# Optimization experiments

Measured on AMD Instinct MI355X. Metric: run time of the kernel, lower is better.

## Reference

```python
import jax, jax.numpy as jnp
import numpy as np

# ---- configuration (from init_kwargs / image geometry) ----
NUM_CLASSES = 10          # digit classes 1..10 (scores has K+1 cols, col 0 = background)
R = 500000                # total digit proposals for the image
T = 2048                  # topk_per_image: fixed-size survivor set for jit-friendly NMS
SCORE_T = 0.05            # digit_score_thresh
NMS_T = 0.5               # nms_thresh
IMG_W, IMG_H = 1920.0, 1080.0
CLS_OFFSET = IMG_W + IMG_H + 1.0  # batched_nms coordinate-offset trick (per-class NMS)


def setup_inputs() -> dict:
    key = jax.random.key(0)
    k1, k2, k3, k4 = jax.random.split(key, 4)
    # realistic boxes: uniform centers over the image, sizes in [10, 100] px
    cxcy = jax.random.uniform(k1, (R, 2)) * jnp.array([IMG_W, IMG_H], dtype=jnp.float32)
    wh = 10.0 + 90.0 * jax.random.uniform(k2, (R, 2))
    boxes = jnp.concatenate([cxcy - 0.5 * wh, cxcy + 0.5 * wh], axis=1)  # [R,4] x1y1x2y2
    # class probabilities over K+1 classes (col 0 = background)
    scores = jax.nn.softmax(jax.random.normal(k3, (R, NUM_CLASSES + 1)), axis=1)
    # per-box digit-center score (pred_digit_center_scores)
    center_scores = jax.random.uniform(k4, (R,))
    return {"boxes": boxes, "scores": scores, "center_scores": center_scores}


def _iou_matrix(b):
    # b: [T,4] in x1y1x2y2. Returns [T,T] pairwise IoU.
    area = jnp.clip(b[:, 2] - b[:, 0], 0.0) * jnp.clip(b[:, 3] - b[:, 1], 0.0)  # [T]
    lt = jnp.maximum(b[:, None, :2], b[None, :, :2])  # [T,T,2]
    rb = jnp.minimum(b[:, None, 2:], b[None, :, 2:])  # [T,T,2]
    wh = jnp.clip(rb - lt, 0.0)
    inter = wh[..., 0] * wh[..., 1]
    return inter / (area[:, None] + area[None, :] - inter + 1e-9)


def reference(boxes, scores, center_scores):
    # 1) drop background column, fuse with digit-center scores
    fg = scores[:, 1:] * center_scores[:, None]            # [R,K]
    # 2) clip boxes to image (Boxes.clip)
    clipped = jnp.stack([
        jnp.clip(boxes[:, 0], 0.0, IMG_W),
        jnp.clip(boxes[:, 1], 0.0, IMG_H),
        jnp.clip(boxes[:, 2], 0.0, IMG_W),
        jnp.clip(boxes[:, 3], 0.0, IMG_H),
    ], axis=1)                                             # [R,4]
    # 3) flatten (box, class) candidates and threshold (filter_mask = scores > thresh)
    flat = fg.reshape(-1)                                  # [R*K]
    masked = jnp.where(flat > SCORE_T, flat, -1.0)
    # 4) fixed-size pre-filter: top-T candidates by fused score
    vals, idx = jax.lax.top_k(masked, T)                   # sorted descending
    cand_boxes = clipped[idx // NUM_CLASSES]               # [T,4]
    cand_cls = idx % NUM_CLASSES                           # [T] (cls_id - 1)
    valid = vals > SCORE_T
    # 5) per-class batched NMS via coordinate-offset trick
    nms_boxes = cand_boxes + cand_cls.astype(cand_boxes.dtype)[:, None] * CLS_OFFSET
    iou = _iou_matrix(nms_boxes)                           # [T,T]
    rng = jnp.arange(T)
    def body(i, keep):
        sup = keep[i] & (iou[i] > NMS_T) & (rng > i)
        return keep & jnp.logical_not(sup)
    keep = jax.lax.fori_loop(0, T, body, valid)            # greedy NMS (inputs sorted by score)
    # 6) masked fixed-shape outputs: kept boxes + kept scores
    out_boxes = jnp.where(keep[:, None], cand_boxes, 0.0)
    out_scores = jnp.where(keep, vals, 0.0)
    return jnp.concatenate([out_boxes, out_scores[:, None]], axis=1)  # [T,5]
```

## Files before the change

kernel.cpp:

```cpp
#include <hip/hip_runtime.h>
#include <stdint.h>

typedef unsigned int u32;
typedef unsigned long long u64;

#define SCORE_THR 0.05f
#define NMS_THR   0.5f
#define TK        2048
#define CAP       4096
#define BASE14    ((int)(0x3D4CCCCDu >> 14))
#define MAGIC11   3123612579ull
#define NREP      8
#define PAIR_CAP  16384
#define SGRID     1024

#define WS_OFFS   0
#define WS_BINPOS 16384
#define WS_HDR    32768
#define WS_CBX    33024
#define WS_NBX    65792
#define WS_VALS   98560
#define WS_HREP   106752
#define WS_BUF    237824
#define WS_PAIRS  269824

__global__ void k_hist(const float* __restrict__ scores,
                       const float* __restrict__ center,
                       int R, u32* __restrict__ hrep) {
    __shared__ u32 h[4096];
    for (int t = threadIdx.x; t < 4096; t += blockDim.x) h[t] = 0;
    __syncthreads();
    int total_e = R * 11;
    int nq = total_e >> 2;
    int qpb = (nq + (int)gridDim.x - 1) / (int)gridDim.x;
    int start = (int)blockIdx.x * qpb;
    int end = start + qpb; if (end > nq) end = nq;
    int bd = (int)blockDim.x;
    for (int q = start + (int)threadIdx.x; q < end; q += 4 * bd) {
        int q1 = q + bd, q2 = q + 2 * bd, q3 = q + 3 * bd;
        float4 va, vb, vc, vd;
        bool ga = true, gb = q1 < end, gc = q2 < end, gd = q3 < end;
        va = ((const float4*)scores)[q];
        if (gb) vb = ((const float4*)scores)[q1];
        if (gc) vc = ((const float4*)scores)[q2];
        if (gd) vd = ((const float4*)scores)[q3];
#define HPROC(g, qq, v4)                                                   \
        if (g) {                                                           \
            float vv[4] = {v4.x, v4.y, v4.z, v4.w};                        \
            _Pragma("unroll")                                              \
            for (int j = 0; j < 4; j++) {                                  \
                u32 e2 = ((u32)(qq) << 2) + (u32)j;                        \
                u32 r = (u32)(((u64)e2 * MAGIC11) >> 35);                  \
                u32 c = e2 - r * 11u;                                      \
                if (c != 0u) {                                             \
                    float s = __fmul_rn(vv[j], center[r]);                 \
                    if (s > SCORE_THR) {                                   \
                        u32 key = __float_as_uint(s);                      \
                        int b = (int)(key >> 14) - BASE14;                 \
                        b = min(max(b, 0), 4095);                          \
                        atomicAdd(&h[b], 1u);                              \
                    }                                                      \
                }                                                          \
            }                                                              \
        }
        HPROC(ga, q, va) HPROC(gb, q1, vb) HPROC(gc, q2, vc) HPROC(gd, q3, vd)
#undef HPROC
    }
    if (blockIdx.x == 0 && threadIdx.x == 0) {
        for (int e2 = nq << 2; e2 < total_e; e2++) {
            u32 r = (u32)(((u64)(u32)e2 * MAGIC11) >> 35);
            u32 c = (u32)e2 - r * 11u;
            if (c != 0u) {
                float s = __fmul_rn(scores[e2], center[r]);
                if (s > SCORE_THR) {
                    u32 key = __float_as_uint(s);
                    int b = (int)(key >> 14) - BASE14;
                    b = min(max(b, 0), 4095);
                    atomicAdd(&h[b], 1u);
                }
            }
        }
    }
    __syncthreads();
    u32* hout = hrep + (size_t)(blockIdx.x & (NREP - 1)) * 4096;
    for (int t = threadIdx.x; t < 4096; t += blockDim.x)
        if (h[t]) atomicAdd(&hout[t], h[t]);
}

__global__ void k_scan(const u32* __restrict__ hrep, u32* __restrict__ offs,
                       u32* hdr) {
    int lane = threadIdx.x;
    int base = 4096 - 64 * (lane + 1);
    u32 v[64];
    u32 segsum = 0;
#pragma unroll
    for (int j = 0; j < 64; j++) {
        u32 s = 0;
#pragma unroll
        for (int i = 0; i < NREP; i++) s += hrep[i * 4096 + base + j];
        v[j] = s; segsum += s;
    }
    u32 incl = segsum;
    for (int off = 1; off < 64; off <<= 1) {
        u32 t = (u32)__shfl_up((int)incl, off);
        if (lane >= off) incl += t;
    }
    u32 excl = incl - segsum;
    u32 total = (u32)__shfl((int)incl, 63);
    u32 run = excl;
#pragma unroll
    for (int j = 63; j >= 0; j--) { offs[base + j] = run; run += v[j]; }
    if (lane == 0) hdr[6] = total;
    if (total < (u32)TK) {
        if (lane == 0) { hdr[3] = 0; hdr[5] = total; }
        return;
    }
    if ((excl < (u32)TK) && (incl >= (u32)TK)) {
        u32 cum = excl;
#pragma unroll
        for (int j = 63; j >= 0; j--) {
            u32 nc = cum + v[j];
            if (nc >= (u32)TK) { hdr[3] = (u32)(base + j); hdr[5] = nc; break; }
            cum = nc;
        }
    }
}

__global__ void k_collect(const float* __restrict__ scores,
                          const float* __restrict__ center,
                          int R, const u32* __restrict__ hdr,
                          const u32* __restrict__ offs, u32* __restrict__ binpos,
                          u64* __restrict__ buf) {
    u32 thr = hdr[3];
    int total_e = R * 11;
    int nq = total_e >> 2;
    int qpb = (nq + (int)gridDim.x - 1) / (int)gridDim.x;
    int start = (int)blockIdx.x * qpb;
    int end = start + qpb; if (end > nq) end = nq;
    int bd = (int)blockDim.x;
    for (int q = start + (int)threadIdx.x; q < end; q += 4 * bd) {
        int q1 = q + bd, q2 = q + 2 * bd, q3 = q + 3 * bd;
        float4 va, vb, vc, vd;
        bool ga = true, gb = q1 < end, gc = q2 < end, gd = q3 < end;
        va = ((const float4*)scores)[q];
        if (gb) vb = ((const float4*)scores)[q1];
        if (gc) vc = ((const float4*)scores)[q2];
        if (gd) vd = ((const float4*)scores)[q3];
#define CPROC(g, qq, v4)                                                   \
        if (g) {                                                           \
            float vv[4] = {v4.x, v4.y, v4.z, v4.w};                        \
            _Pragma("unroll")                                              \
            for (int j = 0; j < 4; j++) {                                  \
                u32 e2 = ((u32)(qq) << 2) + (u32)j;                        \
                u32 r = (u32)(((u64)e2 * MAGIC11) >> 35);                  \
                u32 c = e2 - r * 11u;                                      \
                if (c != 0u) {                                             \
                    float s = __fmul_rn(vv[j], center[r]);                 \
                    if (s > SCORE_THR) {                                   \
                        u32 key = __float_as_uint(s);                      \
                        int b = (int)(key >> 14) - BASE14;                 \
                        b = min(max(b, 0), 4095);                          \
                        if ((u32)b >= thr) {                               \
                            u32 slot = atomicAdd(&binpos[b], 1u);          \
                            u32 pos = offs[b] + slot;                      \
                            if (pos < CAP) {                               \
                                u32 idx = r * 10u + (c - 1u);              \
                                buf[pos] = ((u64)key << 32) | (u64)(~idx); \
                            }                                              \
                        }                                                  \
                    }                                                      \
                }                                                          \
            }                                                              \
        }
        CPROC(ga, q, va) CPROC(gb, q1, vb) CPROC(gc, q2, vc) CPROC(gd, q3, vd)
#undef CPROC
    }
    if (blockIdx.x == 0 && threadIdx.x == 0) {
        for (int e2 = nq << 2; e2 < total_e; e2++) {
            u32 r = (u32)(((u64)(u32)e2 * MAGIC11) >> 35);
            u32 c = (u32)e2 - r * 11u;
            if (c != 0u) {
                float s = __fmul_rn(scores[e2], center[r]);
                if (s > SCORE_THR) {
                    u32 key = __float_as_uint(s);
                    int b = (int)(key >> 14) - BASE14;
                    b = min(max(b, 0), 4095);
                    if ((u32)b >= thr) {
                        u32 slot = atomicAdd(&binpos[b], 1u);
                        u32 pos = offs[b] + slot;
                        if (pos < CAP) {
                            u32 idx = r * 10u + (c - 1u);
                            buf[pos] = ((u64)key << 32) | (u64)(~idx);
                        }
                    }
                }
            }
        }
    }
}

__global__ __launch_bounds__(1024) void k_rank(
        const float* __restrict__ boxes, const u32* __restrict__ offs,
        const u32* __restrict__ hdr, const u64* __restrict__ buf,
        float* __restrict__ cand_bx, float* __restrict__ nms_bx,
        float* __restrict__ vals) {
    __shared__ u64 kb[CAP];
    __shared__ u32 lo[4096];
    int tid = threadIdx.x;
    u32 n = hdr[5]; if (n > (u32)CAP) n = CAP;
    u32 total = hdr[6];
    for (int t = tid; t < CAP; t += 1024) kb[t] = (t < (int)n) ? buf[t] : 0ull;
    for (int t = tid; t < 4096; t += 1024) lo[t] = offs[t];
    __syncthreads();
    for (int i = tid; i < (int)n; i += 1024) {
        u64 x = kb[i];
        u32 key = (u32)(x >> 32);
        int b = (int)(key >> 14) - BASE14;
        b = min(max(b, 0), 4095);
        u32 start = lo[b];
        u32 end = (b > 0) ? lo[b - 1] : total;
        if (end > (u32)CAP) end = CAP;
        u32 rk = start;
        for (u32 j = start; j < end; j++) rk += (kb[j] > x) ? 1u : 0u;
        if (rk < (u32)TK) {
            u32 idx = ~(u32)x;
            u32 r = idx / 10u, cls = idx % 10u;
            const float* bp = boxes + (size_t)r * 4;
            float c0 = fminf(fmaxf(bp[0], 0.f), 1920.f);
            float c1 = fminf(fmaxf(bp[1], 0.f), 1080.f);
            float c2 = fminf(fmaxf(bp[2], 0.f), 1920.f);
            float c3 = fminf(fmaxf(bp[3], 0.f), 1080.f);
            float offv = __fmul_rn((float)cls, 3001.0f);
            cand_bx[rk * 4 + 0] = c0; cand_bx[rk * 4 + 1] = c1;
            cand_bx[rk * 4 + 2] = c2; cand_bx[rk * 4 + 3] = c3;
            nms_bx[rk * 4 + 0] = __fadd_rn(c0, offv);
            nms_bx[rk * 4 + 1] = __fadd_rn(c1, offv);
            nms_bx[rk * 4 + 2] = __fadd_rn(c2, offv);
            nms_bx[rk * 4 + 3] = __fadd_rn(c3, offv);
            vals[rk] = __uint_as_float(key);
        }
    }
}

__global__ void k_mask(const float* __restrict__ nms_bx, u32* __restrict__ hdr,
                       u32* __restrict__ pairs) {
    int colbase = blockIdx.x * 64, rowbase = blockIdx.y * 64;
    if (colbase + 63 <= rowbase) return;
    __shared__ float4 cb[64];
    __shared__ float ca[64];
    int tid = threadIdx.x;
    float4 c = ((const float4*)nms_bx)[colbase + tid];
    cb[tid] = c;
    ca[tid] = __fmul_rn(fmaxf(__fsub_rn(c.z, c.x), 0.f),
                        fmaxf(__fsub_rn(c.w, c.y), 0.f));
    int row = rowbase + tid;
    float4 rb = ((const float4*)nms_bx)[row];
    float rarea = __fmul_rn(fmaxf(__fsub_rn(rb.z, rb.x), 0.f),
                            fmaxf(__fsub_rn(rb.w, rb.y), 0.f));
    __syncthreads();
    for (int cc = 0; cc < 64; cc++) {
        int col = colbase + cc;
        if (col > row) {
            float4 cbv = cb[cc];
            float ltx = fmaxf(rb.x, cbv.x), lty = fmaxf(rb.y, cbv.y);
            float rbx = fminf(rb.z, cbv.z), rby = fminf(rb.w, cbv.w);
            float w = fmaxf(__fsub_rn(rbx, ltx), 0.f);
            float h = fmaxf(__fsub_rn(rby, lty), 0.f);
            float inter = __fmul_rn(w, h);
            float denom = __fadd_rn(__fsub_rn(__fadd_rn(rarea, ca[cc]), inter), 1e-9f);
            float iou = __fdiv_rn(inter, denom);
            if (iou > NMS_THR) {
                u32 p = atomicAdd(&hdr[8], 1u);
                if (p < PAIR_CAP)
                    pairs[p] = ((u32)row << 11) | (u32)col;
            }
        }
    }
}

__global__ __launch_bounds__(64) void k_final(
        const u32* __restrict__ pairs, const u32* __restrict__ hdr,
        const float* __restrict__ vals, const float* __restrict__ cand_bx,
        float* __restrict__ out) {
    __shared__ u32 sp[PAIR_CAP];
    __shared__ u32 cur[2048];
    int lane = threadIdx.x;
    u32 np = hdr[8]; if (np > (u32)PAIR_CAP) np = PAIR_CAP;
    const float4* vp = (const float4*)vals + (size_t)lane * 8;
    float4 vv[8];
#pragma unroll
    for (int j = 0; j < 8; j++) vv[j] = vp[j];
    u32 validw = 0;
#pragma unroll
    for (int j = 0; j < 8; j++) {
        validw |= (vv[j].x > SCORE_THR ? 1u : 0u) << (4 * j + 0);
        validw |= (vv[j].y > SCORE_THR ? 1u : 0u) << (4 * j + 1);
        validw |= (vv[j].z > SCORE_THR ? 1u : 0u) << (4 * j + 2);
        validw |= (vv[j].w > SCORE_THR ? 1u : 0u) << (4 * j + 3);
    }
    for (int t = lane; t < 2048; t += 64) cur[t] = 0;
    __syncthreads();
    for (u32 k = lane; k < np; k += 64) atomicAdd(&cur[pairs[k] >> 11], 1u);
    __syncthreads();
    u32 cnt[32];
    u32 seg = 0;
#pragma unroll
    for (int j = 0; j < 32; j++) { cnt[j] = cur[lane * 32 + j]; seg += cnt[j]; }
    u32 incl = seg;
    for (int off = 1; off < 64; off <<= 1) {
        u32 t = (u32)__shfl_up((int)incl, off);
        if (lane >= off) incl += t;
    }
    u32 run = incl - seg;
#pragma unroll
    for (int j = 0; j < 32; j++) { cur[lane * 32 + j] = run; run += cnt[j]; }
    __syncthreads();
    for (u32 k = lane; k < np; k += 64) {
        u32 p = pairs[k];
        u32 pos = atomicAdd(&cur[p >> 11], 1u);
        sp[pos] = p;
    }
    __syncthreads();
    u32 removed = 0;
    for (u32 k = 0; k < np; k++) {
        u32 p = sp[k];
        u32 row = p >> 11, col = p & 2047u;
        u32 aw = (u32)__shfl((int)(validw & ~removed), (int)(row >> 5));
        if ((aw >> (row & 31)) & 1u)
            if (lane == (int)(col >> 5)) removed |= 1u << (col & 31);
    }
    u32 keepw = validw & ~removed;
#pragma unroll
    for (int b = 0; b < 32; b++) {
        int i = lane * 32 + b;
        bool kp = (keepw >> b) & 1u;
        const float4 bx = ((const float4*)cand_bx)[i];
        float v = (b & 3) == 0 ? vv[b >> 2].x :
                  (b & 3) == 1 ? vv[b >> 2].y :
                  (b & 3) == 2 ? vv[b >> 2].z : vv[b >> 2].w;
        out[i * 5 + 0] = kp ? bx.x : 0.f;
        out[i * 5 + 1] = kp ? bx.y : 0.f;
        out[i * 5 + 2] = kp ? bx.z : 0.f;
        out[i * 5 + 3] = kp ? bx.w : 0.f;
        out[i * 5 + 4] = kp ? v : 0.f;
    }
}

extern "C" void kernel_launch(void* const* d_in, const int* in_sizes, int n_in,
                              void* d_out, int out_size, void* d_ws, size_t ws_size,
                              hipStream_t stream) {
    const float* boxes = (const float*)d_in[0];
    const float* scores = (const float*)d_in[1];
    const float* center = (const float*)d_in[2];
    float* out = (float*)d_out;
    int R = in_sizes[2];

    char* w = (char*)d_ws;
    u32* offs   = (u32*)(w + WS_OFFS);
    u32* binpos = (u32*)(w + WS_BINPOS);
    u32* hdr    = (u32*)(w + WS_HDR);
    float* cbx  = (float*)(w + WS_CBX);
    float* nbx  = (float*)(w + WS_NBX);
    float* vls  = (float*)(w + WS_VALS);
    u32* hrep   = (u32*)(w + WS_HREP);
    u64* buf    = (u64*)(w + WS_BUF);
    u32* pairs  = (u32*)(w + WS_PAIRS);

    hipMemsetAsync(w + WS_BINPOS, 0, WS_BUF - WS_BINPOS, stream);

    k_hist<<<SGRID, 256, 0, stream>>>(scores, center, R, hrep);
    k_scan<<<1, 64, 0, stream>>>(hrep, offs, hdr);
    k_collect<<<SGRID, 256, 0, stream>>>(scores, center, R, hdr, offs, binpos, buf);
    k_rank<<<1, 1024, 0, stream>>>(boxes, offs, hdr, buf, cbx, nbx, vls);
    k_mask<<<dim3(32, 32), 64, 0, stream>>>(nbx, hdr, pairs);
    k_final<<<1, 64, 0, stream>>>(pairs, hdr, vls, cbx, out);
}
```

Before: 141.2 us.

## Spill above-threshold candidates during histogram pass instead of rescanning scores

The histogram kernel now also writes every candidate that passes the score threshold into a per-block spill segment, along with a per-block count. The collect pass then reads only these compacted segments instead of re-reading and re-scoring the full scores and center arrays. This removes a second full pass over the large scores tensor. In exchange it adds global writes and reads of the spilled candidates and a contended shared-memory atomic counter per surviving element. Candidates beyond the per-block capacity are silently dropped, which could lose results on inputs with very dense surviving scores.

```diff
diff --git a/kernel.cpp b/kernel.cpp
--- a/kernel.cpp
+++ b/kernel.cpp
@@ -13,6 +13,7 @@
 #define NREP      8
 #define PAIR_CAP  16384
 #define SGRID     1024
+#define SEGCAP    8192
 
 #define WS_OFFS   0
 #define WS_BINPOS 16384
@@ -23,13 +24,19 @@
 #define WS_HREP   106752
 #define WS_BUF    237824
 #define WS_PAIRS  269824
+#define WS_SCNT   335360
+#define WS_SPILL  339456
 
 __global__ void k_hist(const float* __restrict__ scores,
                        const float* __restrict__ center,
-                       int R, u32* __restrict__ hrep) {
+                       int R, u32* __restrict__ hrep,
+                       u64* __restrict__ spill, u32* __restrict__ scnt) {
     __shared__ u32 h[4096];
+    __shared__ u32 sc;
     for (int t = threadIdx.x; t < 4096; t += blockDim.x) h[t] = 0;
-    __syncthreads();
+    if (threadIdx.x == 0) sc = 0;
+    __syncthreads();
+    u64* seg = spill + (size_t)blockIdx.x * SEGCAP;
     int total_e = R * 11;
     int nq = total_e >> 2;
     int qpb = (nq + (int)gridDim.x - 1) / (int)gridDim.x;
@@ -59,6 +66,10 @@
                         int b = (int)(key >> 14) - BASE14;                 \
                         b = min(max(b, 0), 4095);                          \
                         atomicAdd(&h[b], 1u);                              \
+                        u32 idx = r * 10u + (c - 1u);                      \
+                        u32 pos = atomicAdd(&sc, 1u);                      \
+                        if (pos < SEGCAP)                                  \
+                            seg[pos] = ((u64)key << 32) | (u64)(~idx);     \
                     }                                                      \
                 }                                                          \
             }                                                              \
@@ -77,6 +88,10 @@
                     int b = (int)(key >> 14) - BASE14;
                     b = min(max(b, 0), 4095);
                     atomicAdd(&h[b], 1u);
+                    u32 idx = r * 10u + (c - 1u);
+                    u32 pos = atomicAdd(&sc, 1u);
+                    if (pos < SEGCAP)
+                        seg[pos] = ((u64)key << 32) | (u64)(~idx);
                 }
             }
         }
@@ -85,6 +100,7 @@
     u32* hout = hrep + (size_t)(blockIdx.x & (NREP - 1)) * 4096;
     for (int t = threadIdx.x; t < 4096; t += blockDim.x)
         if (h[t]) atomicAdd(&hout[t], h[t]);
+    if (threadIdx.x == 0) scnt[blockIdx.x] = min(sc, (u32)SEGCAP);
 }
 
 __global__ void k_scan(const u32* __restrict__ hrep, u32* __restrict__ offs,
@@ -126,75 +142,23 @@
     }
 }
 
-__global__ void k_collect(const float* __restrict__ scores,
-                          const float* __restrict__ center,
-                          int R, const u32* __restrict__ hdr,
-                          const u32* __restrict__ offs, u32* __restrict__ binpos,
-                          u64* __restrict__ buf) {
+__global__ void k_collect2(const u64* __restrict__ spill,
+                           const u32* __restrict__ scnt,
+                           const u32* __restrict__ hdr,
+                           const u32* __restrict__ offs, u32* __restrict__ binpos,
+                           u64* __restrict__ buf) {
     u32 thr = hdr[3];
-    int total_e = R * 11;
-    int nq = total_e >> 2;
-    int qpb = (nq + (int)gridDim.x - 1) / (int)gridDim.x;
-    int start = (int)blockIdx.x * qpb;
-    int end = start + qpb; if (end > nq) end = nq;
-    int bd = (int)blockDim.x;
-    for (int q = start + (int)threadIdx.x; q < end; q += 4 * bd) {
-        int q1 = q + bd, q2 = q + 2 * bd, q3 = q + 3 * bd;
-        float4 va, vb, vc, vd;
-        bool ga = true, gb = q1 < end, gc = q2 < end, gd = q3 < end;
-        va = ((const float4*)scores)[q];
-        if (gb) vb = ((const float4*)scores)[q1];
-        if (gc) vc = ((const float4*)scores)[q2];
-        if (gd) vd = ((const float4*)scores)[q3];
-#define CPROC(g, qq, v4)                                                   \
-        if (g) {                                                           \
-            float vv[4] = {v4.x, v4.y, v4.z, v4.w};                        \
-            _Pragma("unroll")                                              \
-            for (int j = 0; j < 4; j++) {                                  \
-                u32 e2 = ((u32)(qq) << 2) + (u32)j;                        \
-                u32 r = (u32)(((u64)e2 * MAGIC11) >> 35);                  \
-                u32 c = e2 - r * 11u;                                      \
-                if (c != 0u) {                                             \
-                    float s = __fmul_rn(vv[j], center[r]);                 \
-                    if (s > SCORE_THR) {                                   \
-                        u32 key = __float_as_uint(s);                      \
-                        int b = (int)(key >> 14) - BASE14;                 \
-                        b = min(max(b, 0), 4095);                          \
-                        if ((u32)b >= thr) {                               \
-                            u32 slot = atomicAdd(&binpos[b], 1u);          \
-                            u32 pos = offs[b] + slot;                      \
-                            if (pos < CAP) {                               \
-                                u32 idx = r * 10u + (c - 1u);              \
-                                buf[pos] = ((u64)key << 32) | (u64)(~idx); \
-                            }                                              \
-                        }                                                  \
-                    }                                                      \
-                }                                                          \
-            }                                                              \
-        }
-        CPROC(ga, q, va) CPROC(gb, q1, vb) CPROC(gc, q2, vc) CPROC(gd, q3, vd)
-#undef CPROC
-    }
-    if (blockIdx.x == 0 && threadIdx.x == 0) {
-        for (int e2 = nq << 2; e2 < total_e; e2++) {
-            u32 r = (u32)(((u64)(u32)e2 * MAGIC11) >> 35);
-            u32 c = (u32)e2 - r * 11u;
-            if (c != 0u) {
-                float s = __fmul_rn(scores[e2], center[r]);
-                if (s > SCORE_THR) {
-                    u32 key = __float_as_uint(s);
-                    int b = (int)(key >> 14) - BASE14;
-                    b = min(max(b, 0), 4095);
-                    if ((u32)b >= thr) {
-                        u32 slot = atomicAdd(&binpos[b], 1u);
-                        u32 pos = offs[b] + slot;
-                        if (pos < CAP) {
-                            u32 idx = r * 10u + (c - 1u);
-                            buf[pos] = ((u64)key << 32) | (u64)(~idx);
-                        }
-                    }
-                }
-            }
+    u32 n = scnt[blockIdx.x];
+    const u64* seg = spill + (size_t)blockIdx.x * SEGCAP;
+    for (u32 i = threadIdx.x; i < n; i += blockDim.x) {
+        u64 v = seg[i];
+        u32 key = (u32)(v >> 32);
+        int b = (int)(key >> 14) - BASE14;
+        b = min(max(b, 0), 4095);
+        if ((u32)b >= thr) {
+            u32 slot = atomicAdd(&binpos[b], 1u);
+            u32 pos = offs[b] + slot;
+            if (pos < CAP) buf[pos] = v;
         }
     }
 }
@@ -365,12 +329,14 @@
     u32* hrep   = (u32*)(w + WS_HREP);
     u64* buf    = (u64*)(w + WS_BUF);
     u32* pairs  = (u32*)(w + WS_PAIRS);
+    u32* scnt   = (u32*)(w + WS_SCNT);
+    u64* spill  = (u64*)(w + WS_SPILL);
 
     hipMemsetAsync(w + WS_BINPOS, 0, WS_BUF - WS_BINPOS, stream);
 
-    k_hist<<<SGRID, 256, 0, stream>>>(scores, center, R, hrep);
+    k_hist<<<SGRID, 256, 0, stream>>>(scores, center, R, hrep, spill, scnt);
     k_scan<<<1, 64, 0, stream>>>(hrep, offs, hdr);
-    k_collect<<<SGRID, 256, 0, stream>>>(scores, center, R, hdr, offs, binpos, buf);
+    k_collect2<<<SGRID, 256, 0, stream>>>(spill, scnt, hdr, offs, binpos, buf);
     k_rank<<<1, 1024, 0, stream>>>(boxes, offs, hdr, buf, cbx, nbx, vls);
     k_mask<<<dim3(32, 32), 64, 0, stream>>>(nbx, hdr, pairs);
     k_final<<<1, 64, 0, stream>>>(pairs, hdr, vls, cbx, out);
```

Result: no change. 142.4 us (+0.8%).

## Fuse pipeline stages via last-block tails and spill high-score candidates during histogram

Applied to the files above, without the earlier changes.

The histogram kernel now also writes candidates above a fixed bin into per-block spill segments, so the collect pass can read those small segments instead of rescanning all scores when the threshold bin is high enough. The scan, rank and final NMS stages are folded into the preceding kernels as last-block-done tails guarded by atomic counters and thread fences, which cuts the launch count from six to three. In exchange, collect now runs with 1024-thread blocks and a large shared footprint on every block. The fallback full rescan also runs with this larger block size, and the tail work is serialized on a single block.

```diff
diff --git a/kernel.cpp b/kernel.cpp
--- a/kernel.cpp
+++ b/kernel.cpp
@@ -9,10 +9,12 @@
 #define TK        2048
 #define CAP       4096
 #define BASE14    ((int)(0x3D4CCCCDu >> 14))
+#define SPILL_BIN 1024
 #define MAGIC11   3123612579ull
 #define NREP      8
 #define PAIR_CAP  16384
 #define SGRID     1024
+#define SEGCAP    8192
 
 #define WS_OFFS   0
 #define WS_BINPOS 16384
@@ -23,20 +25,29 @@
 #define WS_HREP   106752
 #define WS_BUF    237824
 #define WS_PAIRS  269824
+#define WS_SCNT   335360
+#define WS_SPILL  339456
 
 __global__ void k_hist(const float* __restrict__ scores,
                        const float* __restrict__ center,
-                       int R, u32* __restrict__ hrep) {
+                       int R, u32* __restrict__ hrep,
+                       u64* __restrict__ spill, u32* __restrict__ scnt,
+                       u32* __restrict__ offs, u32* __restrict__ hdr) {
     __shared__ u32 h[4096];
-    for (int t = threadIdx.x; t < 4096; t += blockDim.x) h[t] = 0;
-    __syncthreads();
+    __shared__ u32 sc;
+    __shared__ u32 lastblk;
+    int tid = threadIdx.x;
+    for (int t = tid; t < 4096; t += blockDim.x) h[t] = 0;
+    if (tid == 0) sc = 0;
+    __syncthreads();
+    u64* seg = spill + (size_t)blockIdx.x * SEGCAP;
     int total_e = R * 11;
     int nq = total_e >> 2;
     int qpb = (nq + (int)gridDim.x - 1) / (int)gridDim.x;
     int start = (int)blockIdx.x * qpb;
     int end = start + qpb; if (end > nq) end = nq;
     int bd = (int)blockDim.x;
-    for (int q = start + (int)threadIdx.x; q < end; q += 4 * bd) {
+    for (int q = start + tid; q < end; q += 4 * bd) {
         int q1 = q + bd, q2 = q + 2 * bd, q3 = q + 3 * bd;
         float4 va, vb, vc, vd;
         bool ga = true, gb = q1 < end, gc = q2 < end, gd = q3 < end;
@@ -59,6 +70,12 @@
                         int b = (int)(key >> 14) - BASE14;                 \
                         b = min(max(b, 0), 4095);                          \
                         atomicAdd(&h[b], 1u);                              \
+                        if (b >= SPILL_BIN) {                              \
+                            u32 idx = r * 10u + (c - 1u);                  \
+                            u32 pos = atomicAdd(&sc, 1u);                  \
+                            if (pos < SEGCAP)                              \
+                                seg[pos] = ((u64)key << 32) | (u64)(~idx); \
+                        }                                                  \
                     }                                                      \
                 }                                                          \
             }                                                              \
@@ -66,7 +83,7 @@
         HPROC(ga, q, va) HPROC(gb, q1, vb) HPROC(gc, q2, vc) HPROC(gd, q3, vd)
 #undef HPROC
     }
-    if (blockIdx.x == 0 && threadIdx.x == 0) {
+    if (blockIdx.x == 0 && tid == 0) {
         for (int e2 = nq << 2; e2 < total_e; e2++) {
             u32 r = (u32)(((u64)(u32)e2 * MAGIC11) >> 35);
             u32 c = (u32)e2 - r * 11u;
@@ -77,29 +94,42 @@
                     int b = (int)(key >> 14) - BASE14;
                     b = min(max(b, 0), 4095);
                     atomicAdd(&h[b], 1u);
+                    if (b >= SPILL_BIN) {
+                        u32 idx = r * 10u + (c - 1u);
+                        u32 pos = atomicAdd(&sc, 1u);
+                        if (pos < SEGCAP)
+                            seg[pos] = ((u64)key << 32) | (u64)(~idx);
+                    }
                 }
             }
         }
     }
     __syncthreads();
     u32* hout = hrep + (size_t)(blockIdx.x & (NREP - 1)) * 4096;
-    for (int t = threadIdx.x; t < 4096; t += blockDim.x)
+    for (int t = tid; t < 4096; t += blockDim.x)
         if (h[t]) atomicAdd(&hout[t], h[t]);
-}
-
-__global__ void k_scan(const u32* __restrict__ hrep, u32* __restrict__ offs,
-                       u32* hdr) {
-    int lane = threadIdx.x;
+    if (tid == 0) {
+        scnt[blockIdx.x] = min(sc, (u32)SEGCAP);
+        if (sc > (u32)SEGCAP) atomicOr(&hdr[13], 1u);
+    }
+    __threadfence();
+    __syncthreads();
+    if (tid == 0) lastblk = atomicAdd(&hdr[9], 1u);
+    __syncthreads();
+    if (lastblk != gridDim.x - 1) return;
+    __threadfence();
+    for (int t = tid; t < 4096; t += blockDim.x) {
+        u32 s = 0;
+#pragma unroll
+        for (int i = 0; i < NREP; i++) s += atomicOr(&hrep[i * 4096 + t], 0u);
+        h[t] = s;
+    }
+    __syncthreads();
+    if (tid >= 64) return;
+    int lane = tid;
     int base = 4096 - 64 * (lane + 1);
-    u32 v[64];
     u32 segsum = 0;
-#pragma unroll
-    for (int j = 0; j < 64; j++) {
-        u32 s = 0;
-#pragma unroll
-        for (int i = 0; i < NREP; i++) s += hrep[i * 4096 + base + j];
-        v[j] = s; segsum += s;
-    }
+    for (int j = 0; j < 64; j++) segsum += h[base + j];
     u32 incl = segsum;
     for (int off = 1; off < 64; off <<= 1) {
         u32 t = (u32)__shfl_up((int)incl, off);
@@ -108,8 +138,7 @@
     u32 excl = incl - segsum;
     u32 total = (u32)__shfl((int)incl, 63);
     u32 run = excl;
-#pragma unroll
-    for (int j = 63; j >= 0; j--) { offs[base + j] = run; run += v[j]; }
+    for (int j = 63; j >= 0; j--) { u32 hv = h[base + j]; offs[base + j] = run; run += hv; }
     if (lane == 0) hdr[6] = total;
     if (total < (u32)TK) {
         if (lane == 0) { hdr[3] = 0; hdr[5] = total; }
@@ -117,99 +146,120 @@
     }
     if ((excl < (u32)TK) && (incl >= (u32)TK)) {
         u32 cum = excl;
-#pragma unroll
         for (int j = 63; j >= 0; j--) {
-            u32 nc = cum + v[j];
+            u32 hv = h[base + j];
+            u32 nc = cum + hv;
             if (nc >= (u32)TK) { hdr[3] = (u32)(base + j); hdr[5] = nc; break; }
             cum = nc;
         }
     }
 }
 
-__global__ void k_collect(const float* __restrict__ scores,
-                          const float* __restrict__ center,
-                          int R, const u32* __restrict__ hdr,
-                          const u32* __restrict__ offs, u32* __restrict__ binpos,
-                          u64* __restrict__ buf) {
+__global__ __launch_bounds__(1024) void k_collect(
+        const float* __restrict__ scores, const float* __restrict__ center,
+        int R, const u64* __restrict__ spill, const u32* __restrict__ scnt,
+        const u32* __restrict__ offs, u32* __restrict__ hdr,
+        u32* __restrict__ binpos, u64* __restrict__ buf,
+        const float* __restrict__ boxes, float* __restrict__ cand_bx,
+        float* __restrict__ nms_bx, float* __restrict__ vals) {
+    __shared__ u64 kb[CAP];
+    __shared__ u32 lo[4096];
+    __shared__ u32 lastblk;
+    int tid = threadIdx.x;
     u32 thr = hdr[3];
-    int total_e = R * 11;
-    int nq = total_e >> 2;
-    int qpb = (nq + (int)gridDim.x - 1) / (int)gridDim.x;
-    int start = (int)blockIdx.x * qpb;
-    int end = start + qpb; if (end > nq) end = nq;
-    int bd = (int)blockDim.x;
-    for (int q = start + (int)threadIdx.x; q < end; q += 4 * bd) {
-        int q1 = q + bd, q2 = q + 2 * bd, q3 = q + 3 * bd;
-        float4 va, vb, vc, vd;
-        bool ga = true, gb = q1 < end, gc = q2 < end, gd = q3 < end;
-        va = ((const float4*)scores)[q];
-        if (gb) vb = ((const float4*)scores)[q1];
-        if (gc) vc = ((const float4*)scores)[q2];
-        if (gd) vd = ((const float4*)scores)[q3];
+    bool pathA = (thr >= (u32)SPILL_BIN) && (hdr[13] == 0u);
+    if (pathA) {
+        u32 n = scnt[blockIdx.x];
+        const u64* seg = spill + (size_t)blockIdx.x * SEGCAP;
+        for (u32 i = tid; i < n; i += blockDim.x) {
+            u64 v = seg[i];
+            u32 key = (u32)(v >> 32);
+            int b = (int)(key >> 14) - BASE14;
+            b = min(max(b, 0), 4095);
+            if ((u32)b >= thr) {
+                u32 slot = atomicAdd(&binpos[b], 1u);
+                u32 pos = offs[b] + slot;
+                if (pos < CAP) buf[pos] = v;
+            }
+        }
+    } else {
+        int total_e = R * 11;
+        int nq = total_e >> 2;
+        int qpb = (nq + (int)gridDim.x - 1) / (int)gridDim.x;
+        int start = (int)blockIdx.x * qpb;
+        int end = start + qpb; if (end > nq) end = nq;
+        int bd = (int)blockDim.x;
+        for (int q = start + tid; q < end; q += 4 * bd) {
+            int q1 = q + bd, q2 = q + 2 * bd, q3 = q + 3 * bd;
+            float4 va, vb, vc, vd;
+            bool ga = true, gb = q1 < end, gc = q2 < end, gd = q3 < end;
+            va = ((const float4*)scores)[q];
+            if (gb) vb = ((const float4*)scores)[q1];
+            if (gc) vc = ((const float4*)scores)[q2];
+            if (gd) vd = ((const float4*)scores)[q3];
 #define CPROC(g, qq, v4)                                                   \
-        if (g) {                                                           \
-            float vv[4] = {v4.x, v4.y, v4.z, v4.w};                        \
-            _Pragma("unroll")                                              \
-            for (int j = 0; j < 4; j++) {                                  \
-                u32 e2 = ((u32)(qq) << 2) + (u32)j;                        \
-                u32 r = (u32)(((u64)e2 * MAGIC11) >> 35);                  \
-                u32 c = e2 - r * 11u;                                      \
-                if (c != 0u) {                                             \
-                    float s = __fmul_rn(vv[j], center[r]);                 \
-                    if (s > SCORE_THR) {                                   \
-                        u32 key = __float_as_uint(s);                      \
-                        int b = (int)(key >> 14) - BASE14;                 \
-                        b = min(max(b, 0), 4095);                          \
-                        if ((u32)b >= thr) {                               \
-                            u32 slot = atomicAdd(&binpos[b], 1u);          \
-                            u32 pos = offs[b] + slot;                      \
-                            if (pos < CAP) {                               \
-                                u32 idx = r * 10u + (c - 1u);              \
-                                buf[pos] = ((u64)key << 32) | (u64)(~idx); \
+            if (g) {                                                       \
+                float vv[4] = {v4.x, v4.y, v4.z, v4.w};                    \
+                _Pragma("unroll")                                          \
+                for (int j = 0; j < 4; j++) {                              \
+                    u32 e2 = ((u32)(qq) << 2) + (u32)j;                    \
+                    u32 r = (u32)(((u64)e2 * MAGIC11) >> 35);              \
+                    u32 c = e2 - r * 11u;                                  \
+                    if (c != 0u) {                                         \
+                        float s = __fmul_rn(vv[j], center[r]);             \
+                        if (s > SCORE_THR) {                               \
+                            u32 key = __float_as_uint(s);                  \
+                            int b = (int)(key >> 14) - BASE14;             \
+                            b = min(max(b, 0), 4095);                      \
+                            if ((u32)b >= thr) {                           \
+                                u32 slot = atomicAdd(&binpos[b], 1u);      \
+                                u32 pos = offs[b] + slot;                  \
+                                if (pos < CAP) {                           \
+                                    u32 idx = r * 10u + (c - 1u);          \
+                                    buf[pos] = ((u64)key << 32) |          \
+                                               (u64)(~idx);               \
+                                }                                          \
                             }                                              \
                         }                                                  \
                     }                                                      \
                 }                                                          \
-            }                                                              \
-        }
-        CPROC(ga, q, va) CPROC(gb, q1, vb) CPROC(gc, q2, vc) CPROC(gd, q3, vd)
+            }
+            CPROC(ga, q, va) CPROC(gb, q1, vb) CPROC(gc, q2, vc) CPROC(gd, q3, vd)
 #undef CPROC
-    }
-    if (blockIdx.x == 0 && threadIdx.x == 0) {
-        for (int e2 = nq << 2; e2 < total_e; e2++) {
-            u32 r = (u32)(((u64)(u32)e2 * MAGIC11) >> 35);
-            u32 c = (u32)e2 - r * 11u;
-            if (c != 0u) {
-                float s = __fmul_rn(scores[e2], center[r]);
-                if (s > SCORE_THR) {
-                    u32 key = __float_as_uint(s);
-                    int b = (int)(key >> 14) - BASE14;
-                    b = min(max(b, 0), 4095);
-                    if ((u32)b >= thr) {
-                        u32 slot = atomicAdd(&binpos[b], 1u);
-                        u32 pos = offs[b] + slot;
-                        if (pos < CAP) {
-                            u32 idx = r * 10u + (c - 1u);
-                            buf[pos] = ((u64)key << 32) | (u64)(~idx);
+        }
+        if (blockIdx.x == 0 && tid == 0) {
+            for (int e2 = nq << 2; e2 < total_e; e2++) {
+                u32 r = (u32)(((u64)(u32)e2 * MAGIC11) >> 35);
+                u32 c = (u32)e2 - r * 11u;
+                if (c != 0u) {
+                    float s = __fmul_rn(scores[e2], center[r]);
+                    if (s > SCORE_THR) {
+                        u32 key = __float_as_uint(s);
+                        int b = (int)(key >> 14) - BASE14;
+                        b = min(max(b, 0), 4095);
+                        if ((u32)b >= thr) {
+                            u32 slot = atomicAdd(&binpos[b], 1u);
+                            u32 pos = offs[b] + slot;
+                            if (pos < CAP) {
+                                u32 idx = r * 10u + (c - 1u);
+                                buf[pos] = ((u64)key << 32) | (u64)(~idx);
+                            }
                         }
                     }
                 }
             }
         }
     }
-}
-
-__global__ __launch_bounds__(1024) void k_rank(
-        const float* __restrict__ boxes, const u32* __restrict__ offs,
-        const u32* __restrict__ hdr, const u64* __restrict__ buf,
-        float* __restrict__ cand_bx, float* __restrict__ nms_bx,
-        float* __restrict__ vals) {
-    __shared__ u64 kb[CAP];
-    __shared__ u32 lo[4096];
-    int tid = threadIdx.x;
+    __threadfence();
+    __syncthreads();
+    if (tid == 0) lastblk = atomicAdd(&hdr[10], 1u);
+    __syncthreads();
+    if (lastblk != gridDim.x - 1) return;
+    __threadfence();
     u32 n = hdr[5]; if (n > (u32)CAP) n = CAP;
     u32 total = hdr[6];
-    for (int t = tid; t < CAP; t += 1024) kb[t] = (t < (int)n) ? buf[t] : 0ull;
+    for (int t = tid; t < CAP; t += 1024)
+        kb[t] = (t < (int)n) ? atomicOr((u64*)&buf[t], 0ull) : 0ull;
     for (int t = tid; t < 4096; t += 1024) lo[t] = offs[t];
     __syncthreads();
     for (int i = tid; i < (int)n; i += 1024) {
@@ -242,50 +292,55 @@
     }
 }
 
-__global__ void k_mask(const float* __restrict__ nms_bx, u32* __restrict__ hdr,
-                       u32* __restrict__ pairs) {
-    int colbase = blockIdx.x * 64, rowbase = blockIdx.y * 64;
-    if (colbase + 63 <= rowbase) return;
+__global__ __launch_bounds__(64) void k_mask(
+        const float* __restrict__ nms_bx, u32* __restrict__ hdr,
+        u32* __restrict__ pairs, const float* __restrict__ vals,
+        const float* __restrict__ cand_bx, float* __restrict__ out) {
     __shared__ float4 cb[64];
     __shared__ float ca[64];
-    int tid = threadIdx.x;
-    float4 c = ((const float4*)nms_bx)[colbase + tid];
-    cb[tid] = c;
-    ca[tid] = __fmul_rn(fmaxf(__fsub_rn(c.z, c.x), 0.f),
-                        fmaxf(__fsub_rn(c.w, c.y), 0.f));
-    int row = rowbase + tid;
-    float4 rb = ((const float4*)nms_bx)[row];
-    float rarea = __fmul_rn(fmaxf(__fsub_rn(rb.z, rb.x), 0.f),
-                            fmaxf(__fsub_rn(rb.w, rb.y), 0.f));
-    __syncthreads();
-    for (int cc = 0; cc < 64; cc++) {
-        int col = colbase + cc;
-        if (col > row) {
-            float4 cbv = cb[cc];
-            float ltx = fmaxf(rb.x, cbv.x), lty = fmaxf(rb.y, cbv.y);
-            float rbx = fminf(rb.z, cbv.z), rby = fminf(rb.w, cbv.w);
-            float w = fmaxf(__fsub_rn(rbx, ltx), 0.f);
-            float h = fmaxf(__fsub_rn(rby, lty), 0.f);
-            float inter = __fmul_rn(w, h);
-            float denom = __fadd_rn(__fsub_rn(__fadd_rn(rarea, ca[cc]), inter), 1e-9f);
-            float iou = __fdiv_rn(inter, denom);
-            if (iou > NMS_THR) {
-                u32 p = atomicAdd(&hdr[8], 1u);
-                if (p < PAIR_CAP)
-                    pairs[p] = ((u32)row << 11) | (u32)col;
-            }
-        }
-    }
-}
-
-__global__ __launch_bounds__(64) void k_final(
-        const u32* __restrict__ pairs, const u32* __restrict__ hdr,
-        const float* __restrict__ vals, const float* __restrict__ cand_bx,
-        float* __restrict__ out) {
     __shared__ u32 sp[PAIR_CAP];
     __shared__ u32 cur[2048];
-    int lane = threadIdx.x;
-    u32 np = hdr[8]; if (np > (u32)PAIR_CAP) np = PAIR_CAP;
+    __shared__ u32 lastblk;
+    int tid = threadIdx.x;
+    int colbase = blockIdx.x * 64, rowbase = blockIdx.y * 64;
+    if (colbase + 63 > rowbase) {
+        float4 c = ((const float4*)nms_bx)[colbase + tid];
+        cb[tid] = c;
+        ca[tid] = __fmul_rn(fmaxf(__fsub_rn(c.z, c.x), 0.f),
+                            fmaxf(__fsub_rn(c.w, c.y), 0.f));
+        int row = rowbase + tid;
+        float4 rb = ((const float4*)nms_bx)[row];
+        float rarea = __fmul_rn(fmaxf(__fsub_rn(rb.z, rb.x), 0.f),
+                                fmaxf(__fsub_rn(rb.w, rb.y), 0.f));
+        __syncthreads();
+        for (int cc = 0; cc < 64; cc++) {
+            int col = colbase + cc;
+            if (col > row) {
+                float4 cbv = cb[cc];
+                float ltx = fmaxf(rb.x, cbv.x), lty = fmaxf(rb.y, cbv.y);
+                float rbx = fminf(rb.z, cbv.z), rby = fminf(rb.w, cbv.w);
+                float w = fmaxf(__fsub_rn(rbx, ltx), 0.f);
+                float h = fmaxf(__fsub_rn(rby, lty), 0.f);
+                float inter = __fmul_rn(w, h);
+                float denom = __fadd_rn(__fsub_rn(__fadd_rn(rarea, ca[cc]), inter), 1e-9f);
+                float iou = __fdiv_rn(inter, denom);
+                if (iou > NMS_THR) {
+                    u32 p = atomicAdd(&hdr[8], 1u);
+                    if (p < PAIR_CAP)
+                        pairs[p] = ((u32)row << 11) | (u32)col;
+                }
+            }
+        }
+    }
+    __threadfence();
+    __syncthreads();
+    if (tid == 0) lastblk = atomicAdd(&hdr[11], 1u);
+    __syncthreads();
+    u32 nblk = gridDim.x * gridDim.y;
+    if (lastblk != nblk - 1) return;
+    __threadfence();
+    int lane = tid;
+    u32 np = atomicOr(&hdr[8], 0u); if (np > (u32)PAIR_CAP) np = PAIR_CAP;
     const float4* vp = (const float4*)vals + (size_t)lane * 8;
     float4 vv[8];
 #pragma unroll
@@ -300,7 +355,8 @@
     }
     for (int t = lane; t < 2048; t += 64) cur[t] = 0;
     __syncthreads();
-    for (u32 k = lane; k < np; k += 64) atomicAdd(&cur[pairs[k] >> 11], 1u);
+    for (u32 k = lane; k < np; k += 64)
+        atomicAdd(&cur[atomicOr(&pairs[k], 0u) >> 11], 1u);
     __syncthreads();
     u32 cnt[32];
     u32 seg = 0;
@@ -316,7 +372,7 @@
     for (int j = 0; j < 32; j++) { cur[lane * 32 + j] = run; run += cnt[j]; }
     __syncthreads();
     for (u32 k = lane; k < np; k += 64) {
-        u32 p = pairs[k];
+        u32 p = atomicOr(&pairs[k], 0u);
         u32 pos = atomicAdd(&cur[p >> 11], 1u);
         sp[pos] = p;
     }
@@ -365,13 +421,14 @@
     u32* hrep   = (u32*)(w + WS_HREP);
     u64* buf    = (u64*)(w + WS_BUF);
     u32* pairs  = (u32*)(w + WS_PAIRS);
+    u32* scnt   = (u32*)(w + WS_SCNT);
+    u64* spill  = (u64*)(w + WS_SPILL);
 
     hipMemsetAsync(w + WS_BINPOS, 0, WS_BUF - WS_BINPOS, stream);
 
-    k_hist<<<SGRID, 256, 0, stream>>>(scores, center, R, hrep);
-    k_scan<<<1, 64, 0, stream>>>(hrep, offs, hdr);
-    k_collect<<<SGRID, 256, 0, stream>>>(scores, center, R, hdr, offs, binpos, buf);
-    k_rank<<<1, 1024, 0, stream>>>(boxes, offs, hdr, buf, cbx, nbx, vls);
-    k_mask<<<dim3(32, 32), 64, 0, stream>>>(nbx, hdr, pairs);
-    k_final<<<1, 64, 0, stream>>>(pairs, hdr, vls, cbx, out);
+    k_hist<<<SGRID, 256, 0, stream>>>(scores, center, R, hrep, spill, scnt,
+                                      offs, hdr);
+    k_collect<<<SGRID, 1024, 0, stream>>>(scores, center, R, spill, scnt, offs,
+                                          hdr, binpos, buf, boxes, cbx, nbx, vls);
+    k_mask<<<dim3(32, 32), 64, 0, stream>>>(nbx, hdr, pairs, vls, cbx, out);
 }
```

Result: slower. 450.3 us (+218.8%).

## Stream scores once into per-block spill of high-score candidates, reuse for hist/collect

Applied to the files above, without the earlier changes.

Adds a first streaming pass that reads the 22 MB score tensor once and writes only candidates with fused score at or above a fixed high key (about 0.2) into per-block spill segments. When the spill holds at least TK candidates and no segment overflowed, the histogram and collect kernels work only on the small spill lists instead of rescanning the full input. Otherwise they fall back to the original full scans. This cuts two full input passes down to one, at the cost of an extra kernel launch, global spill writes and a data-dependent fallback. NREP is also reduced from 8 to 4.

```diff
diff --git a/kernel.cpp b/kernel.cpp
--- a/kernel.cpp
+++ b/kernel.cpp
@@ -9,10 +9,13 @@
 #define TK        2048
 #define CAP       4096
 #define BASE14    ((int)(0x3D4CCCCDu >> 14))
+#define SPILL_BIN 1024
+#define SPILL_KEY 0x3E4CC000u
 #define MAGIC11   3123612579ull
-#define NREP      8
+#define NREP      4
 #define PAIR_CAP  16384
 #define SGRID     1024
+#define SEGCAP    1024
 
 #define WS_OFFS   0
 #define WS_BINPOS 16384
@@ -21,22 +24,110 @@
 #define WS_NBX    65792
 #define WS_VALS   98560
 #define WS_HREP   106752
-#define WS_BUF    237824
-#define WS_PAIRS  269824
-
-__global__ void k_hist(const float* __restrict__ scores,
-                       const float* __restrict__ center,
-                       int R, u32* __restrict__ hrep) {
-    __shared__ u32 h[4096];
-    for (int t = threadIdx.x; t < 4096; t += blockDim.x) h[t] = 0;
-    __syncthreads();
+#define WS_BUF    172288
+#define WS_PAIRS  204672
+#define WS_SCNT   270208
+#define WS_SPILL  274304
+
+__global__ void k_stream(const float* __restrict__ scores,
+                         const float* __restrict__ center,
+                         int R, u64* __restrict__ spill, u32* __restrict__ scnt,
+                         u32* __restrict__ hdr) {
+    __shared__ u32 sc;
+    int tid = threadIdx.x;
+    if (tid == 0) sc = 0;
+    __syncthreads();
+    u64* seg = spill + (size_t)blockIdx.x * SEGCAP;
     int total_e = R * 11;
     int nq = total_e >> 2;
     int qpb = (nq + (int)gridDim.x - 1) / (int)gridDim.x;
     int start = (int)blockIdx.x * qpb;
     int end = start + qpb; if (end > nq) end = nq;
     int bd = (int)blockDim.x;
-    for (int q = start + (int)threadIdx.x; q < end; q += 4 * bd) {
+    for (int q = start + tid; q < end; q += 4 * bd) {
+        int q1 = q + bd, q2 = q + 2 * bd, q3 = q + 3 * bd;
+        float4 va, vb, vc, vd;
+        bool ga = true, gb = q1 < end, gc = q2 < end, gd = q3 < end;
+        va = ((const float4*)scores)[q];
+        if (gb) vb = ((const float4*)scores)[q1];
+        if (gc) vc = ((const float4*)scores)[q2];
+        if (gd) vd = ((const float4*)scores)[q3];
+#define SPROC(g, qq, v4)                                                   \
+        if (g) {                                                           \
+            float vv[4] = {v4.x, v4.y, v4.z, v4.w};                        \
+            _Pragma("unroll")                                              \
+            for (int j = 0; j < 4; j++) {                                  \
+                u32 e2 = ((u32)(qq) << 2) + (u32)j;                        \
+                u32 r = (u32)(((u64)e2 * MAGIC11) >> 35);                  \
+                u32 c = e2 - r * 11u;                                      \
+                if (c != 0u) {                                             \
+                    float s = __fmul_rn(vv[j], center[r]);                 \
+                    u32 key = __float_as_uint(s);                          \
+                    if (key >= SPILL_KEY) {                                \
+                        u32 idx = r * 10u + (c - 1u);                      \
+                        u32 pos = atomicAdd(&sc, 1u);                      \
+                        if (pos < SEGCAP)                                  \
+                            seg[pos] = ((u64)key << 32) | (u64)(~idx);     \
+                    }                                                      \
+                }                                                          \
+            }                                                              \
+        }
+        SPROC(ga, q, va) SPROC(gb, q1, vb) SPROC(gc, q2, vc) SPROC(gd, q3, vd)
+#undef SPROC
+    }
+    if (blockIdx.x == 0 && tid == 0) {
+        for (int e2 = nq << 2; e2 < total_e; e2++) {
+            u32 r = (u32)(((u64)(u32)e2 * MAGIC11) >> 35);
+            u32 c = (u32)e2 - r * 11u;
+            if (c != 0u) {
+                float s = __fmul_rn(scores[e2], center[r]);
+                u32 key = __float_as_uint(s);
+                if (key >= SPILL_KEY) {
+                    u32 idx = r * 10u + (c - 1u);
+                    u32 pos = atomicAdd(&sc, 1u);
+                    if (pos < SEGCAP)
+                        seg[pos] = ((u64)key << 32) | (u64)(~idx);
+                }
+            }
+        }
+    }
+    __syncthreads();
+    if (tid == 0) {
+        u32 m = min(sc, (u32)SEGCAP);
+        scnt[blockIdx.x] = m;
+        atomicAdd(&hdr[12], m);
+        if (sc > (u32)SEGCAP) atomicOr(&hdr[13], 1u);
+    }
+}
+
+__global__ void k_hist(const float* __restrict__ scores,
+                       const float* __restrict__ center, int R,
+                       const u64* __restrict__ spill, const u32* __restrict__ scnt,
+                       const u32* __restrict__ hdr, u32* __restrict__ hrep) {
+    bool happy = (hdr[12] >= (u32)TK) && (hdr[13] == 0u);
+    if (happy) {
+        u32 n = scnt[blockIdx.x];
+        const u64* seg = spill + (size_t)blockIdx.x * SEGCAP;
+        u32* hout = hrep + (size_t)(blockIdx.x & (NREP - 1)) * 4096;
+        for (u32 i = threadIdx.x; i < n; i += blockDim.x) {
+            u32 key = (u32)(seg[i] >> 32);
+            int b = (int)(key >> 14) - BASE14;
+            b = min(max(b, 0), 4095);
+            atomicAdd(&hout[b], 1u);
+        }
+        return;
+    }
+    __shared__ u32 h[4096];
+    int tid = threadIdx.x;
+    for (int t = tid; t < 4096; t += blockDim.x) h[t] = 0;
+    __syncthreads();
+    int total_e = R * 11;
+    int nq = total_e >> 2;
+    int qpb = (nq + (int)gridDim.x - 1) / (int)gridDim.x;
+    int start = (int)blockIdx.x * qpb;
+    int end = start + qpb; if (end > nq) end = nq;
+    int bd = (int)blockDim.x;
+    for (int q = start + tid; q < end; q += 4 * bd) {
         int q1 = q + bd, q2 = q + 2 * bd, q3 = q + 3 * bd;
         float4 va, vb, vc, vd;
         bool ga = true, gb = q1 < end, gc = q2 < end, gd = q3 < end;
@@ -66,7 +157,7 @@
         HPROC(ga, q, va) HPROC(gb, q1, vb) HPROC(gc, q2, vc) HPROC(gd, q3, vd)
 #undef HPROC
     }
-    if (blockIdx.x == 0 && threadIdx.x == 0) {
+    if (blockIdx.x == 0 && tid == 0) {
         for (int e2 = nq << 2; e2 < total_e; e2++) {
             u32 r = (u32)(((u64)(u32)e2 * MAGIC11) >> 35);
             u32 c = (u32)e2 - r * 11u;
@@ -83,7 +174,7 @@
     }
     __syncthreads();
     u32* hout = hrep + (size_t)(blockIdx.x & (NREP - 1)) * 4096;
-    for (int t = threadIdx.x; t < 4096; t += blockDim.x)
+    for (int t = tid; t < 4096; t += blockDim.x)
         if (h[t]) atomicAdd(&hout[t], h[t]);
 }
 
@@ -127,18 +218,36 @@
 }
 
 __global__ void k_collect(const float* __restrict__ scores,
-                          const float* __restrict__ center,
-                          int R, const u32* __restrict__ hdr,
-                          const u32* __restrict__ offs, u32* __restrict__ binpos,
-                          u64* __restrict__ buf) {
+                          const float* __restrict__ center, int R,
+                          const u64* __restrict__ spill, const u32* __restrict__ scnt,
+                          const u32* __restrict__ hdr, const u32* __restrict__ offs,
+                          u32* __restrict__ binpos, u64* __restrict__ buf) {
     u32 thr = hdr[3];
+    bool happy = (hdr[12] >= (u32)TK) && (hdr[13] == 0u);
+    if (happy) {
+        u32 n = scnt[blockIdx.x];
+        const u64* seg = spill + (size_t)blockIdx.x * SEGCAP;
+        for (u32 i = threadIdx.x; i < n; i += blockDim.x) {
+            u64 v = seg[i];
+            u32 key = (u32)(v >> 32);
+            int b = (int)(key >> 14) - BASE14;
+            b = min(max(b, 0), 4095);
+            if ((u32)b >= thr) {
+                u32 slot = atomicAdd(&binpos[b], 1u);
+                u32 pos = offs[b] + slot;
+                if (pos < CAP) buf[pos] = v;
+            }
+        }
+        return;
+    }
     int total_e = R * 11;
     int nq = total_e >> 2;
     int qpb = (nq + (int)gridDim.x - 1) / (int)gridDim.x;
     int start = (int)blockIdx.x * qpb;
     int end = start + qpb; if (end > nq) end = nq;
     int bd = (int)blockDim.x;
-    for (int q = start + (int)threadIdx.x; q < end; q += 4 * bd) {
+    int tid = threadIdx.x;
+    for (int q = start + tid; q < end; q += 4 * bd) {
         int q1 = q + bd, q2 = q + 2 * bd, q3 = q + 3 * bd;
         float4 va, vb, vc, vd;
         bool ga = true, gb = q1 < end, gc = q2 < end, gd = q3 < end;
@@ -175,7 +284,7 @@
         CPROC(ga, q, va) CPROC(gb, q1, vb) CPROC(gc, q2, vc) CPROC(gd, q3, vd)
 #undef CPROC
     }
-    if (blockIdx.x == 0 && threadIdx.x == 0) {
+    if (blockIdx.x == 0 && tid == 0) {
         for (int e2 = nq << 2; e2 < total_e; e2++) {
             u32 r = (u32)(((u64)(u32)e2 * MAGIC11) >> 35);
             u32 c = (u32)e2 - r * 11u;
@@ -365,12 +474,16 @@
     u32* hrep   = (u32*)(w + WS_HREP);
     u64* buf    = (u64*)(w + WS_BUF);
     u32* pairs  = (u32*)(w + WS_PAIRS);
+    u32* scnt   = (u32*)(w + WS_SCNT);
+    u64* spill  = (u64*)(w + WS_SPILL);
 
     hipMemsetAsync(w + WS_BINPOS, 0, WS_BUF - WS_BINPOS, stream);
 
-    k_hist<<<SGRID, 256, 0, stream>>>(scores, center, R, hrep);
+    k_stream<<<SGRID, 256, 0, stream>>>(scores, center, R, spill, scnt, hdr);
+    k_hist<<<SGRID, 256, 0, stream>>>(scores, center, R, spill, scnt, hdr, hrep);
     k_scan<<<1, 64, 0, stream>>>(hrep, offs, hdr);
-    k_collect<<<SGRID, 256, 0, stream>>>(scores, center, R, hdr, offs, binpos, buf);
+    k_collect<<<SGRID, 256, 0, stream>>>(scores, center, R, spill, scnt, hdr,
+                                         offs, binpos, buf);
     k_rank<<<1, 1024, 0, stream>>>(boxes, offs, hdr, buf, cbx, nbx, vls);
     k_mask<<<dim3(32, 32), 64, 0, stream>>>(nbx, hdr, pairs);
     k_final<<<1, 64, 0, stream>>>(pairs, hdr, vls, cbx, out);
```

After: 161.3 us. +14.2%, slower.
